# Optimization experiments

Measured on AMD Instinct MI355X. Metric: run time of the kernel, lower is better.

## Reference

```python
import jax, jax.numpy as jnp
import numpy as np
from itertools import permutations

NODE, BATCH, DIM, STEP = 32, 64, 32, 8
E = NODE * (NODE - 1)          # 992 directed edges (all ordered pairs)
K = 3                          # edge types
MSG_HID = 64; MSG_OUT = 64; N_HID = 64; PRED_LEN = 8


def setup_inputs() -> dict:
    key = jax.random.key(0)
    ks = jax.random.split(key, 12)
    es = jnp.asarray(np.array(list(permutations(range(NODE), 2))).T, dtype=jnp.int32)  # [2, E]
    x = jax.random.normal(ks[0], (BATCH, NODE, DIM, STEP), jnp.float32)
    z = jax.nn.softmax(jax.random.normal(ks[1], (BATCH, E, K), jnp.float32), axis=-1)
    p = lambda k, shape: jax.random.normal(k, shape, jnp.float32) * 0.1
    return dict(
        x=x, z=z, es=es,
        nodes_mask=jnp.zeros((NODE,), jnp.float32),
        edges_mask=jnp.zeros((E,), jnp.float32),
        mask=jnp.zeros((1,), jnp.float32),
        msg_W1=p(ks[2], (K, 2 * DIM, MSG_HID)), msg_b1=jnp.zeros((K, MSG_HID), jnp.float32),
        msg_W2=p(ks[3], (K, MSG_HID, MSG_OUT)), msg_b2=jnp.zeros((K, MSG_OUT), jnp.float32),
        out_W1=p(ks[4], (DIM + MSG_OUT, N_HID)), out_b1=jnp.zeros((N_HID,), jnp.float32),
        out_W2=p(ks[5], (N_HID, N_HID)), out_b2=jnp.zeros((N_HID,), jnp.float32),
        out_W3=p(ks[6], (N_HID, DIM)), out_b3=jnp.zeros((DIM,), jnp.float32),
        ge_Wi=p(ks[7], (3, N_HID, N_HID)), ge_bi=jnp.zeros((3, N_HID), jnp.float32),
        ge_Wh=p(ks[8], (3, N_HID, N_HID)), ge_bh=jnp.zeros((3, N_HID), jnp.float32),
        gn_Wi=p(ks[9], (3, N_HID + DIM, N_HID + DIM)), gn_bi=jnp.zeros((3, N_HID + DIM), jnp.float32),
        gn_Wh=p(ks[10], (3, N_HID + DIM, N_HID + DIM)), gn_bh=jnp.zeros((3, N_HID + DIM), jnp.float32),
    )


def _gru(inp, hid, Wi, bi, Wh, bh):
    # GRUX: state defaults to hidden
    r = jax.nn.sigmoid(inp @ Wi[0] + bi[0] + hid @ Wh[0] + bh[0])
    i = jax.nn.sigmoid(inp @ Wi[1] + bi[1] + hid @ Wh[1] + bh[1])
    n = jnp.tanh(inp @ Wi[2] + bi[2] + r * (hid @ Wh[2] + bh[2]))
    return (1.0 - i) * n + i * hid


def _run(x, z, es, msg_W1, msg_b1, msg_W2, msg_b2,
         out_W1, out_b1, out_W2, out_b2, out_W3, out_b3,
         ge_Wi, ge_bi, ge_Wh, ge_bh, gn_Wi, gn_bi, gn_Wh, gn_bh):
    xp = jnp.transpose(x, (1, 0, 3, 2))   # [node, batch, step, dim]
    zp = jnp.transpose(z, (1, 0, 2))      # [E, batch, K]
    col, row = es[0], es[1]               # 'o2i': col,row = es; aggregate at col
    counts = jnp.clip(jax.ops.segment_sum(jnp.ones((E,), x.dtype), col, num_segments=NODE), 1.0)
    h_node = h_edge = None
    x_m = None
    xs = []
    for t in range(STEP + PRED_LEN):
        x_in = xp[:, :, t, :] if t < STEP else x_m   # [node, batch, dim]
        # edge gather: msg = cat([x[row], x[col]])
        msg = jnp.concatenate([x_in[row], x_in[col]], axis=-1)  # [E, b, 2*dim]
        # per-edge-type 2-layer MLP mixture, weighted by z, normalized by K
        h1 = jax.nn.relu(jnp.einsum('ebi,kih->kebh', msg, msg_W1) + msg_b1[:, None, None, :])
        h2 = jax.nn.relu(jnp.einsum('kebh,kho->kebo', h1, msg_W2) + msg_b2[:, None, None, :])
        msgs = jnp.einsum('kebo,ebk->ebo', h2, zp) / K          # [E, b, msg_out]
        if h_edge is not None:
            msgs = _gru(msgs, h_edge, ge_Wi, ge_bi, ge_Wh, ge_bh)
        # scatter-mean to nodes
        agg = jax.ops.segment_sum(msgs, col, num_segments=NODE) / counts[:, None, None]
        cat = jnp.concatenate([x_in, agg], axis=-1)             # [node, b, dim+msg_out]
        if h_node is not None:
            cat = _gru(cat, h_node, gn_Wi, gn_bi, gn_Wh, gn_bh)
        h = jax.nn.relu(cat @ out_W1 + out_b1)
        h = jax.nn.relu(h @ out_W2 + out_b2)
        delta = h @ out_W3 + out_b3
        x_m = x_in + delta
        h_node, h_edge = cat, msgs
        xs.append(x_m)
    x_hat = jnp.transpose(jnp.stack(xs, axis=2), (1, 0, 3, 2))  # [batch, node, dim, T]
    return x_hat


def reference(x, z, es, nodes_mask, edges_mask, mask,
              msg_W1, msg_b1, msg_W2, msg_b2,
              out_W1, out_b1, out_W2, out_b2, out_W3, out_b3,
              ge_Wi, ge_bi, ge_Wh, ge_bh, gn_Wi, gn_bi, gn_Wh, gn_bh):
    x_hat = _run(x, z, es, msg_W1, msg_b1, msg_W2, msg_b2,
                 out_W1, out_b1, out_W2, out_b2, out_W3, out_b3,
                 ge_Wi, ge_bi, ge_Wh, ge_bh, gn_Wi, gn_bi, gn_Wh, gn_bh)
    return (x_hat[:, :, :, -PRED_LEN:], x_hat, x_hat)
```

## Files before the change

### kernel.cpp

```cpp
#include <hip/hip_runtime.h>
#include <hip/hip_bf16.h>

#define NNODE 32
#define NB    64
#define NDIM  32
#define NSTEP 8
#define NE    992
#define NTT   16

typedef __bf16 bf16;
typedef __attribute__((ext_vector_type(8))) __bf16 bf16x8;
typedef __attribute__((ext_vector_type(4))) __bf16 bf16x4;
typedef __attribute__((ext_vector_type(4))) float  f32x4;

__device__ __forceinline__ f32x4 mfma_bf16(bf16x8 a, bf16x8 b, f32x4 c) {
  return __builtin_amdgcn_mfma_f32_16x16x32_bf16(a, b, c, 0, 0, 0);
}
__device__ __forceinline__ float sigm(float x) { return 1.0f / (1.0f + __expf(-x)); }
__device__ __forceinline__ float tanh_f(float x) {
  x = fminf(fmaxf(x, -15.0f), 15.0f);
  float e = __expf(2.0f * x);
  return (e - 1.0f) / (e + 1.0f);
}

__global__ void prep_weights(
    const float* __restrict__ msgW1, const float* __restrict__ msgW2,
    const float* __restrict__ geWi,  const float* __restrict__ geWh,
    const float* __restrict__ gnWi,  const float* __restrict__ gnWh,
    const float* __restrict__ oW1,   const float* __restrict__ oW2,
    const float* __restrict__ oW3,
    bf16* __restrict__ B1, bf16* __restrict__ B2,
    bf16* __restrict__ GI, bf16* __restrict__ GH,
    bf16* __restrict__ GN,
    bf16* __restrict__ OW1s, bf16* __restrict__ OW2s, bf16* __restrict__ OW3s) {
  int u = blockIdx.x * 256 + threadIdx.x;
  if (u < 12288) {
    int k = u >> 12, i = (u >> 6) & 63, h = u & 63;
    int kf = i >> 5, quad = (i >> 3) & 3, j = i & 7;
    int nn = k * 64 + h, nt = nn >> 4, lane = quad * 16 + (nn & 15);
    int slot = ((nt * 2 + kf) * 64 + lane) * 8 + j;
    B1[slot] = (bf16)msgW1[u];
    GI[slot] = (bf16)geWi[u];
    GH[slot] = (bf16)geWh[u];
    int ntl = h >> 4, lane2 = quad * 16 + (h & 15);
    int slot2 = k * 4096 + ((ntl * 2 + kf) * 64 + lane2) * 8 + j;
    B2[slot2] = (bf16)msgW2[u];
  } else if (u < 39936) {
    int v = u - 12288;
    int kk = v / 9216, rem = v % 9216, i = rem / 96, h = rem % 96;
    int kf = i >> 5, loc = i & 31, quad = loc >> 3, j = loc & 7;
    int nn = kk * 96 + h, nt = nn >> 4, lane = quad * 16 + (nn & 15);
    int slot = ((nt * 3 + kf) * 64 + lane) * 8 + j;
    GN[slot]         = (bf16)gnWi[v];
    GN[27648 + slot] = (bf16)gnWh[v];
  } else if (u < 46080) {
    int v = u - 39936; int i = v >> 6, h = v & 63;
    int kf = i >> 5, loc = i & 31, quad = loc >> 3, j = loc & 7;
    int nt = h >> 4, lane = quad * 16 + (h & 15);
    OW1s[((nt * 3 + kf) * 64 + lane) * 8 + j] = (bf16)oW1[v];
  } else if (u < 50176) {
    int v = u - 46080; int i = v >> 6, h = v & 63;
    int kf = i >> 5, quad = (i >> 3) & 3, j = i & 7;
    int nt = h >> 4, lane = quad * 16 + (h & 15);
    OW2s[((nt * 2 + kf) * 64 + lane) * 8 + j] = (bf16)oW2[v];
  } else if (u < 52224) {
    int v = u - 50176; int i = v >> 5, h = v & 31;
    int kf = i >> 5, quad = (i >> 3) & 3, j = i & 7;
    int nt = h >> 4, lane = quad * 16 + (h & 15);
    OW3s[((nt * 2 + kf) * 64 + lane) * 8 + j] = (bf16)oW3[v];
  }
}

__global__ void copy_x(const float* __restrict__ x, float* __restrict__ xf,
                       bf16* __restrict__ xb) {
  int u = blockIdx.x * 256 + threadIdx.x;
  int n = u >> 11, b = (u >> 5) & 63, d = u & 31;
  float v = x[((b * 32 + n) * 32 + d) * 8 + 0];
  xf[u] = v;
  xb[u] = (bf16)v;
}

__global__ __launch_bounds__(256, 2) void edge_step(
    const bf16* __restrict__ xb, const int* __restrict__ es,
    const float* __restrict__ z,
    const bf16* __restrict__ B1, const bf16* __restrict__ B2,
    const float* __restrict__ mb1, const float* __restrict__ mb2,
    const bf16* __restrict__ GI, const bf16* __restrict__ GH,
    const float* __restrict__ gbi, const float* __restrict__ gbh,
    bf16* __restrict__ hed, int t) {
  __shared__ __align__(16) char scrbuf[51200];
  __shared__ float zL[2][64][3];
  __shared__ float biasL[768];
  bf16 (*A)[64][72]   = (bf16(*)[64][72])scrbuf;
  bf16 (*A2)[64][200] = (bf16(*)[64][200])scrbuf;

  int e0 = blockIdx.x * 2, tid = threadIdx.x;
  int c0_ = es[e0],     r0 = es[NE + e0];
  int c1_ = es[e0 + 1], r1 = es[NE + e0 + 1];
  for (int u = tid; u < 768; u += 256)
    biasL[u] = (u < 192) ? mb1[u] : (u < 384) ? mb2[u - 192]
             : (u < 576) ? gbi[u - 384] : gbh[u - 576];
  for (int u = tid; u < 384; u += 256) {
    int pe = u / 192, rem = u % 192, b = rem / 3, k = rem % 3;
    zL[pe][b][k] = z[(b * NE + e0 + pe) * 3 + k];
  }
  for (int u = tid; u < 1024; u += 256) {
    int pe = u >> 9, c = u & 511;
    int b = c >> 3, i8 = c & 7;
    int nrow = pe ? r1 : r0, ncol = pe ? c1_ : c0_;
    const bf16* src = (i8 < 4) ? (xb + nrow * 2048 + b * 32 + i8 * 8)
                               : (xb + ncol * 2048 + b * 32 + (i8 - 4) * 8);
    *(bf16x8*)&A[pe][b][i8 * 8] = *(const bf16x8*)src;
  }
  __syncthreads();
  int wv = tid >> 6, ln = tid & 63, quad = ln >> 4, l16 = ln & 15;
  int m = wv * 16 + l16;
  bf16x8 af[2][2];
#pragma unroll
  for (int pe = 0; pe < 2; pe++)
#pragma unroll
    for (int kf = 0; kf < 2; kf++)
      af[pe][kf] = *(const bf16x8*)&A[pe][m][kf * 32 + quad * 8];
  __syncthreads();
  f32x4 acc[2][12];
#pragma unroll
  for (int pe = 0; pe < 2; pe++)
#pragma unroll
    for (int q = 0; q < 12; q++) { f32x4 zz = {0.f,0.f,0.f,0.f}; acc[pe][q] = zz; }
#pragma unroll
  for (int nt = 0; nt < 12; nt++) {
    bf16x8 w0 = *(const bf16x8*)&B1[(nt * 2 + 0) * 512 + ln * 8];
    bf16x8 w1 = *(const bf16x8*)&B1[(nt * 2 + 1) * 512 + ln * 8];
#pragma unroll
    for (int pe = 0; pe < 2; pe++) {
      acc[pe][nt] = mfma_bf16(af[pe][0], w0, acc[pe][nt]);
      acc[pe][nt] = mfma_bf16(af[pe][1], w1, acc[pe][nt]);
    }
  }
#pragma unroll
  for (int nt = 0; nt < 12; nt++) {
    int n = nt * 16 + l16;
    float bias = biasL[n];
#pragma unroll
    for (int pe = 0; pe < 2; pe++)
#pragma unroll
      for (int r = 0; r < 4; r++) {
        float v = acc[pe][nt][r] + bias;
        A2[pe][wv * 16 + quad * 4 + r][n] = (bf16)(v > 0.f ? v : 0.f);
      }
  }
  __syncthreads();
  bf16x8 a2[2][3][2];
#pragma unroll
  for (int pe = 0; pe < 2; pe++)
#pragma unroll
    for (int kt = 0; kt < 3; kt++)
#pragma unroll
      for (int kf = 0; kf < 2; kf++)
        a2[pe][kt][kf] = *(const bf16x8*)&A2[pe][m][kt * 64 + kf * 32 + quad * 8];
  __syncthreads();
  f32x4 acc2[2][12];
#pragma unroll
  for (int pe = 0; pe < 2; pe++)
#pragma unroll
    for (int q = 0; q < 12; q++) { f32x4 zz = {0.f,0.f,0.f,0.f}; acc2[pe][q] = zz; }
#pragma unroll
  for (int kt = 0; kt < 3; kt++)
#pragma unroll
    for (int nt = 0; nt < 4; nt++) {
      bf16x8 w0 = *(const bf16x8*)&B2[kt * 4096 + (nt * 2 + 0) * 512 + ln * 8];
      bf16x8 w1 = *(const bf16x8*)&B2[kt * 4096 + (nt * 2 + 1) * 512 + ln * 8];
#pragma unroll
      for (int pe = 0; pe < 2; pe++) {
        acc2[pe][kt * 4 + nt] = mfma_bf16(a2[pe][kt][0], w0, acc2[pe][kt * 4 + nt]);
        acc2[pe][kt * 4 + nt] = mfma_bf16(a2[pe][kt][1], w1, acc2[pe][kt * 4 + nt]);
      }
    }
#pragma unroll
  for (int pe = 0; pe < 2; pe++)
#pragma unroll
    for (int r = 0; r < 4; r++) {
      int b = wv * 16 + quad * 4 + r;
      float z0 = zL[pe][b][0], z1 = zL[pe][b][1], z2 = zL[pe][b][2];
#pragma unroll
      for (int nt = 0; nt < 4; nt++) {
        int o = nt * 16 + l16;
        float h0 = acc2[pe][nt][r]     + biasL[192 + o];       h0 = h0 > 0.f ? h0 : 0.f;
        float h1 = acc2[pe][4 + nt][r] + biasL[192 + 64 + o];  h1 = h1 > 0.f ? h1 : 0.f;
        float h2 = acc2[pe][8 + nt][r] + biasL[192 + 128 + o]; h2 = h2 > 0.f ? h2 : 0.f;
        A[pe][b][o] = (bf16)((h0 * z0 + h1 * z1 + h2 * z2) * (1.0f / 3.0f));
      }
    }
  if (t > 0) {
    __syncthreads();
    bf16x8 ai[2][2], ah[2][2];
#pragma unroll
    for (int pe = 0; pe < 2; pe++) {
      const bf16* hrow = hed + (e0 + pe) * 4096 + m * 64;
#pragma unroll
      for (int kf = 0; kf < 2; kf++) {
        ai[pe][kf] = *(const bf16x8*)&A[pe][m][kf * 32 + quad * 8];
        ah[pe][kf] = *(const bf16x8*)(hrow + kf * 32 + quad * 8);
      }
    }
    f32x4 gri[2][8], gni[2][4], gnh[2][4];
#pragma unroll
    for (int pe = 0; pe < 2; pe++) {
#pragma unroll
      for (int q = 0; q < 8; q++) { f32x4 zz = {0.f,0.f,0.f,0.f}; gri[pe][q] = zz; }
#pragma unroll
      for (int q = 0; q < 4; q++) { f32x4 zz = {0.f,0.f,0.f,0.f}; gni[pe][q] = zz; gnh[pe][q] = zz; }
    }
#pragma unroll
    for (int nt = 0; nt < 8; nt++) {
      bf16x8 wi0 = *(const bf16x8*)&GI[(nt * 2 + 0) * 512 + ln * 8];
      bf16x8 wi1 = *(const bf16x8*)&GI[(nt * 2 + 1) * 512 + ln * 8];
      bf16x8 wh0 = *(const bf16x8*)&GH[(nt * 2 + 0) * 512 + ln * 8];
      bf16x8 wh1 = *(const bf16x8*)&GH[(nt * 2 + 1) * 512 + ln * 8];
#pragma unroll
      for (int pe = 0; pe < 2; pe++) {
        gri[pe][nt] = mfma_bf16(ai[pe][0], wi0, gri[pe][nt]);
        gri[pe][nt] = mfma_bf16(ai[pe][1], wi1, gri[pe][nt]);
        gri[pe][nt] = mfma_bf16(ah[pe][0], wh0, gri[pe][nt]);
        gri[pe][nt] = mfma_bf16(ah[pe][1], wh1, gri[pe][nt]);
      }
    }
#pragma unroll
    for (int nt = 8; nt < 12; nt++) {
      bf16x8 wi0 = *(const bf16x8*)&GI[(nt * 2 + 0) * 512 + ln * 8];
      bf16x8 wi1 = *(const bf16x8*)&GI[(nt * 2 + 1) * 512 + ln * 8];
      bf16x8 wh0 = *(const bf16x8*)&GH[(nt * 2 + 0) * 512 + ln * 8];
      bf16x8 wh1 = *(const bf16x8*)&GH[(nt * 2 + 1) * 512 + ln * 8];
#pragma unroll
      for (int pe = 0; pe < 2; pe++) {
        gni[pe][nt - 8] = mfma_bf16(ai[pe][0], wi0, gni[pe][nt - 8]);
        gni[pe][nt - 8] = mfma_bf16(ai[pe][1], wi1, gni[pe][nt - 8]);
        gnh[pe][nt - 8] = mfma_bf16(ah[pe][0], wh0, gnh[pe][nt - 8]);
        gnh[pe][nt - 8] = mfma_bf16(ah[pe][1], wh1, gnh[pe][nt - 8]);
      }
    }
#pragma unroll
    for (int pe = 0; pe < 2; pe++)
#pragma unroll
      for (int r = 0; r < 4; r++) {
        int b = wv * 16 + quad * 4 + r;
#pragma unroll
        for (int nt = 0; nt < 4; nt++) {
          int o = nt * 16 + l16;
          float xr = gri[pe][nt][r]     + biasL[384 + o]      + biasL[576 + o];
          float xi = gri[pe][4 + nt][r] + biasL[384 + 64 + o] + biasL[576 + 64 + o];
          float xn = gni[pe][nt][r] + biasL[384 + 128 + o];
          float hn = gnh[pe][nt][r] + biasL[576 + 128 + o];
          float rg = sigm(xr);
          float ig = sigm(xi);
          float ng = tanh_f(xn + rg * hn);
          float hv = (float)hed[(e0 + pe) * 4096 + b * 64 + o];
          A[pe][b][o] = (bf16)((1.0f - ig) * ng + ig * hv);
        }
      }
  }
  __syncthreads();
  for (int u = tid; u < 1024; u += 256) {
    int pe = u >> 9, c = u & 511;
    int b = c >> 3, j = c & 7;
    *(bf16x8*)(hed + (e0 + pe) * 4096 + b * 64 + j * 8) = *(const bf16x8*)&A[pe][b][j * 8];
  }
}

__global__ __launch_bounds__(256) void node_kernel(
    const float* __restrict__ x, const bf16* __restrict__ hed,
    float* __restrict__ xf, bf16* __restrict__ xb, float* __restrict__ hnode,
    const bf16* __restrict__ GN,
    const float* __restrict__ gnbi, const float* __restrict__ gnbh,
    const bf16* __restrict__ OW1, const float* __restrict__ ob1,
    const bf16* __restrict__ OW2, const float* __restrict__ ob2,
    const bf16* __restrict__ OW3, const float* __restrict__ ob3,
    float* __restrict__ out, int t) {
  __shared__ float aggf[16][64];
  __shared__ float xinf[16][32];
  __shared__ float hvf[16][96];
  __shared__ __align__(16) bf16 c0b[16][112];
  __shared__ __align__(16) bf16 hvb[16][112];
  __shared__ float gsum[2][16][290];
  __shared__ __align__(16) bf16 cnb[16][112];
  __shared__ __align__(16) bf16 s1b[16][112];
  __shared__ __align__(16) bf16 s2b[16][112];
  int nq = blockIdx.x, n = nq >> 2, q = nq & 3;
  int tid = threadIdx.x;
  {
    int r = tid >> 4, o4 = tid & 15;
    const bf16x4* bp = (const bf16x4*)hed + (size_t)n * 31 * 1024 + (q * 16 + r) * 16 + o4;
    float sx = 0.f, sy = 0.f, sz = 0.f, sw = 0.f;
#pragma unroll
    for (int e2 = 0; e2 < 31; e2++) {
      bf16x4 v = bp[e2 * 1024];
      sx += (float)v[0]; sy += (float)v[1]; sz += (float)v[2]; sw += (float)v[3];
    }
    const float inv = 1.0f / 31.0f;
    sx *= inv; sy *= inv; sz *= inv; sw *= inv;
    int o = o4 * 4;
    aggf[r][o] = sx; aggf[r][o + 1] = sy; aggf[r][o + 2] = sz; aggf[r][o + 3] = sw;
    c0b[r][32 + o] = (bf16)sx; c0b[r][33 + o] = (bf16)sy;
    c0b[r][34 + o] = (bf16)sz; c0b[r][35 + o] = (bf16)sw;
  }
  if (tid < 128) {
    int r = tid >> 3, d0 = (tid & 7) * 4;
    int b = q * 16 + r;
#pragma unroll
    for (int k = 0; k < 4; k++) {
      float v = xf[n * 2048 + b * 32 + d0 + k];
      xinf[r][d0 + k] = v;
      c0b[r][d0 + k] = (bf16)v;
    }
  }
  if (t > 0) {
    int r = tid >> 4, cb = (tid & 15) * 6;
    int row = n * 64 + q * 16 + r;
#pragma unroll
    for (int k = 0; k < 6; k++) {
      float v = hnode[row * 96 + cb + k];
      hvf[r][cb + k] = v;
      hvb[r][cb + k] = (bf16)v;
    }
  }
  __syncthreads();
  int wv = tid >> 6, ln = tid & 63, quad = ln >> 4, l16 = ln & 15;
  if (t > 0) {
    int mat = wv >> 1, sel = wv & 1;
    const bf16(*Ab)[112] = mat ? hvb : c0b;
    bf16x8 af[3];
#pragma unroll
    for (int kf = 0; kf < 3; kf++)
      af[kf] = *(const bf16x8*)&Ab[l16][kf * 32 + quad * 8];
    const bf16* W = GN + mat * 27648;
    f32x4 accn[9];
#pragma unroll
    for (int q2 = 0; q2 < 9; q2++) { f32x4 zz = {0.f,0.f,0.f,0.f}; accn[q2] = zz; }
#pragma unroll
    for (int nt2 = 0; nt2 < 9; nt2++) {
      int nt = sel * 9 + nt2;
#pragma unroll
      for (int kf = 0; kf < 3; kf++) {
        bf16x8 bfrag = *(const bf16x8*)&W[((nt * 3 + kf) * 64 + ln) * 8];
        accn[nt2] = mfma_bf16(af[kf], bfrag, accn[nt2]);
      }
    }
#pragma unroll
    for (int nt2 = 0; nt2 < 9; nt2++) {
      int col = (sel * 9 + nt2) * 16 + l16;
#pragma unroll
      for (int rr = 0; rr < 4; rr++)
        gsum[mat][quad * 4 + rr][col] = accn[nt2][rr];
    }
  }
  __syncthreads();
  {
    int r = tid >> 4, cb = (tid & 15) * 6;
    int row = n * 64 + q * 16 + r;
#pragma unroll
    for (int k = 0; k < 6; k++) {
      int c = cb + k;
      float v;
      if (t > 0) {
        float xr = gsum[0][r][c] + gnbi[c] + gsum[1][r][c] + gnbh[c];
        float xi = gsum[0][r][96 + c] + gnbi[96 + c] + gsum[1][r][96 + c] + gnbh[96 + c];
        float xn = gsum[0][r][192 + c] + gnbi[192 + c];
        float hn = gsum[1][r][192 + c] + gnbh[192 + c];
        float rg = sigm(xr);
        float ig = sigm(xi);
        float ng = tanh_f(xn + rg * hn);
        v = (1.0f - ig) * ng + ig * hvf[r][c];
      } else {
        v = (c < 32) ? xinf[r][c] : aggf[r][c - 32];
      }
      cnb[r][c] = (bf16)v;
      hnode[row * 96 + c] = v;
    }
  }
  __syncthreads();
  {
    bf16x8 af[3];
#pragma unroll
    for (int kf = 0; kf < 3; kf++)
      af[kf] = *(const bf16x8*)&cnb[l16][kf * 32 + quad * 8];
    f32x4 accn = {0.f, 0.f, 0.f, 0.f};
#pragma unroll
    for (int kf = 0; kf < 3; kf++) {
      bf16x8 bfrag = *(const bf16x8*)&OW1[((wv * 3 + kf) * 64 + ln) * 8];
      accn = mfma_bf16(af[kf], bfrag, accn);
    }
    int col = wv * 16 + l16;
    float bias = ob1[col];
#pragma unroll
    for (int rr = 0; rr < 4; rr++) {
      float vv = accn[rr] + bias;
      s1b[quad * 4 + rr][col] = (bf16)(vv > 0.f ? vv : 0.f);
    }
  }
  __syncthreads();
  {
    bf16x8 af[2];
#pragma unroll
    for (int kf = 0; kf < 2; kf++)
      af[kf] = *(const bf16x8*)&s1b[l16][kf * 32 + quad * 8];
    f32x4 accn = {0.f, 0.f, 0.f, 0.f};
#pragma unroll
    for (int kf = 0; kf < 2; kf++) {
      bf16x8 bfrag = *(const bf16x8*)&OW2[((wv * 2 + kf) * 64 + ln) * 8];
      accn = mfma_bf16(af[kf], bfrag, accn);
    }
    int col = wv * 16 + l16;
    float bias = ob2[col];
#pragma unroll
    for (int rr = 0; rr < 4; rr++) {
      float vv = accn[rr] + bias;
      s2b[quad * 4 + rr][col] = (bf16)(vv > 0.f ? vv : 0.f);
    }
  }
  __syncthreads();
  if (wv < 2) {
    bf16x8 af[2];
#pragma unroll
    for (int kf = 0; kf < 2; kf++)
      af[kf] = *(const bf16x8*)&s2b[l16][kf * 32 + quad * 8];
    f32x4 accn = {0.f, 0.f, 0.f, 0.f};
#pragma unroll
    for (int kf = 0; kf < 2; kf++) {
      bf16x8 bfrag = *(const bf16x8*)&OW3[((wv * 2 + kf) * 64 + ln) * 8];
      accn = mfma_bf16(af[kf], bfrag, accn);
    }
    int d = wv * 16 + l16;
    float bias = ob3[d];
#pragma unroll
    for (int rr = 0; rr < 4; rr++) {
      int r = quad * 4 + rr;
      int b = q * 16 + r;
      float xm = xinf[r][d] + accn[rr] + bias;
      int base = (b * 32 + n) * 32 + d;
      out[524288 + base * 16 + t] = xm;
      out[1572864 + base * 16 + t] = xm;
      if (t >= NSTEP) out[base * 8 + (t - NSTEP)] = xm;
      float vnext = (t + 1 < NSTEP) ? x[base * 8 + (t + 1)] : xm;
      xf[n * 2048 + b * 32 + d] = vnext;
      xb[n * 2048 + b * 32 + d] = (bf16)vnext;
    }
  }
}

extern "C" void kernel_launch(void* const* d_in, const int* in_sizes, int n_in,
                              void* d_out, int out_size, void* d_ws, size_t ws_size,
                              hipStream_t stream) {
  const float* x     = (const float*)d_in[0];
  const float* z     = (const float*)d_in[1];
  const int*   es    = (const int*)d_in[2];
  const float* msgW1 = (const float*)d_in[6];
  const float* msgb1 = (const float*)d_in[7];
  const float* msgW2 = (const float*)d_in[8];
  const float* msgb2 = (const float*)d_in[9];
  const float* oW1   = (const float*)d_in[10];
  const float* ob1   = (const float*)d_in[11];
  const float* oW2   = (const float*)d_in[12];
  const float* ob2   = (const float*)d_in[13];
  const float* oW3   = (const float*)d_in[14];
  const float* ob3   = (const float*)d_in[15];
  const float* geWi  = (const float*)d_in[16];
  const float* gebi  = (const float*)d_in[17];
  const float* geWh  = (const float*)d_in[18];
  const float* gebh  = (const float*)d_in[19];
  const float* gnWi  = (const float*)d_in[20];
  const float* gnbi  = (const float*)d_in[21];
  const float* gnWh  = (const float*)d_in[22];
  const float* gnbh  = (const float*)d_in[23];
  float* out = (float*)d_out;

  char* p = (char*)d_ws;
  bf16*  hed   = (bf16*)p;   p += (size_t)NE * 4096 * 2;
  float* xf    = (float*)p;  p += 65536 * 4;
  bf16*  xb    = (bf16*)p;   p += 65536 * 2;
  float* hnode = (float*)p;  p += 196608 * 4;
  bf16*  B1sw  = (bf16*)p;   p += 12288 * 2;
  bf16*  B2sw  = (bf16*)p;   p += 12288 * 2;
  bf16*  GIsw  = (bf16*)p;   p += 12288 * 2;
  bf16*  GHsw  = (bf16*)p;   p += 12288 * 2;
  bf16*  GNsw  = (bf16*)p;   p += 55296 * 2;
  bf16*  OW1s  = (bf16*)p;   p += 6144 * 2;
  bf16*  OW2s  = (bf16*)p;   p += 4096 * 2;
  bf16*  OW3s  = (bf16*)p;   p += 2048 * 2;

  prep_weights<<<204, 256, 0, stream>>>(msgW1, msgW2, geWi, geWh, gnWi, gnWh,
                                        oW1, oW2, oW3,
                                        B1sw, B2sw, GIsw, GHsw, GNsw,
                                        OW1s, OW2s, OW3s);
  copy_x<<<256, 256, 0, stream>>>(x, xf, xb);

  for (int t = 0; t < NTT; t++) {
    edge_step<<<NE / 2, 256, 0, stream>>>(xb, es, z, B1sw, B2sw, msgb1, msgb2,
                                          GIsw, GHsw, gebi, gebh, hed, t);
    node_kernel<<<128, 256, 0, stream>>>(x, hed, xf, xb, hnode, GNsw, gnbi, gnbh,
                                         OW1s, ob1, OW2s, ob2, OW3s, ob3,
                                         out, t);
  }
}
```

Baseline: 657.7 us.

## Split edge_step output columns across two wave groups with 512-thread blocks

The edge kernel now runs 8 waves per block instead of 4. Waves are grouped by row (rg) and by column half (cg), and each wave computes half of the output tiles for the message MLP and the edge GRU. This cuts per-wave accumulator registers and serial MFMA chains so more waves can run and hide latency. In exchange, each wave reloads the same A fragments and there is more per-block sync overhead. The launch bound is raised to (512, 4), which constrains registers per thread.

```diff
diff --git a/kernel.cpp b/kernel.cpp
--- a/kernel.cpp
+++ b/kernel.cpp
@@ -80,7 +80,7 @@
   xb[u] = (bf16)v;
 }
 
-__global__ __launch_bounds__(256, 2) void edge_step(
+__global__ __launch_bounds__(512, 4) void edge_step(
     const bf16* __restrict__ xb, const int* __restrict__ es,
     const float* __restrict__ z,
     const bf16* __restrict__ B1, const bf16* __restrict__ B2,
@@ -97,14 +97,14 @@
   int e0 = blockIdx.x * 2, tid = threadIdx.x;
   int c0_ = es[e0],     r0 = es[NE + e0];
   int c1_ = es[e0 + 1], r1 = es[NE + e0 + 1];
-  for (int u = tid; u < 768; u += 256)
+  for (int u = tid; u < 768; u += 512)
     biasL[u] = (u < 192) ? mb1[u] : (u < 384) ? mb2[u - 192]
              : (u < 576) ? gbi[u - 384] : gbh[u - 576];
-  for (int u = tid; u < 384; u += 256) {
+  for (int u = tid; u < 384; u += 512) {
     int pe = u / 192, rem = u % 192, b = rem / 3, k = rem % 3;
     zL[pe][b][k] = z[(b * NE + e0 + pe) * 3 + k];
   }
-  for (int u = tid; u < 1024; u += 256) {
+  for (int u = tid; u < 1024; u += 512) {
     int pe = u >> 9, c = u & 511;
     int b = c >> 3, i8 = c & 7;
     int nrow = pe ? r1 : r0, ncol = pe ? c1_ : c0_;
@@ -114,7 +114,8 @@
   }
   __syncthreads();
   int wv = tid >> 6, ln = tid & 63, quad = ln >> 4, l16 = ln & 15;
-  int m = wv * 16 + l16;
+  int rg = wv & 3, cg = wv >> 2;
+  int m = rg * 16 + l16;
   bf16x8 af[2][2];
 #pragma unroll
   for (int pe = 0; pe < 2; pe++)
@@ -122,72 +123,76 @@
     for (int kf = 0; kf < 2; kf++)
       af[pe][kf] = *(const bf16x8*)&A[pe][m][kf * 32 + quad * 8];
   __syncthreads();
-  f32x4 acc[2][12];
+  f32x4 acc1[2][6];
 #pragma unroll
   for (int pe = 0; pe < 2; pe++)
 #pragma unroll
-    for (int q = 0; q < 12; q++) { f32x4 zz = {0.f,0.f,0.f,0.f}; acc[pe][q] = zz; }
-#pragma unroll
-  for (int nt = 0; nt < 12; nt++) {
+    for (int q = 0; q < 6; q++) { f32x4 zz = {0.f,0.f,0.f,0.f}; acc1[pe][q] = zz; }
+#pragma unroll
+  for (int j = 0; j < 6; j++) {
+    int nt = cg * 6 + j;
     bf16x8 w0 = *(const bf16x8*)&B1[(nt * 2 + 0) * 512 + ln * 8];
     bf16x8 w1 = *(const bf16x8*)&B1[(nt * 2 + 1) * 512 + ln * 8];
 #pragma unroll
     for (int pe = 0; pe < 2; pe++) {
-      acc[pe][nt] = mfma_bf16(af[pe][0], w0, acc[pe][nt]);
-      acc[pe][nt] = mfma_bf16(af[pe][1], w1, acc[pe][nt]);
-    }
-  }
-#pragma unroll
-  for (int nt = 0; nt < 12; nt++) {
+      acc1[pe][j] = mfma_bf16(af[pe][0], w0, acc1[pe][j]);
+      acc1[pe][j] = mfma_bf16(af[pe][1], w1, acc1[pe][j]);
+    }
+  }
+#pragma unroll
+  for (int j = 0; j < 6; j++) {
+    int nt = cg * 6 + j;
     int n = nt * 16 + l16;
     float bias = biasL[n];
 #pragma unroll
     for (int pe = 0; pe < 2; pe++)
 #pragma unroll
       for (int r = 0; r < 4; r++) {
-        float v = acc[pe][nt][r] + bias;
-        A2[pe][wv * 16 + quad * 4 + r][n] = (bf16)(v > 0.f ? v : 0.f);
-      }
-  }
-  __syncthreads();
-  bf16x8 a2[2][3][2];
+        float v = acc1[pe][j][r] + bias;
+        A2[pe][rg * 16 + quad * 4 + r][n] = (bf16)(v > 0.f ? v : 0.f);
+      }
+  }
+  __syncthreads();
+  f32x4 acc2[2][3][2];
 #pragma unroll
   for (int pe = 0; pe < 2; pe++)
 #pragma unroll
     for (int kt = 0; kt < 3; kt++)
 #pragma unroll
+      for (int oi = 0; oi < 2; oi++) { f32x4 zz = {0.f,0.f,0.f,0.f}; acc2[pe][kt][oi] = zz; }
+#pragma unroll
+  for (int kt = 0; kt < 3; kt++) {
+    bf16x8 a2f[2][2];
+#pragma unroll
+    for (int pe = 0; pe < 2; pe++)
+#pragma unroll
       for (int kf = 0; kf < 2; kf++)
-        a2[pe][kt][kf] = *(const bf16x8*)&A2[pe][m][kt * 64 + kf * 32 + quad * 8];
-  __syncthreads();
-  f32x4 acc2[2][12];
+        a2f[pe][kf] = *(const bf16x8*)&A2[pe][m][kt * 64 + kf * 32 + quad * 8];
+#pragma unroll
+    for (int oi = 0; oi < 2; oi++) {
+      int ot = cg * 2 + oi;
+      bf16x8 w0 = *(const bf16x8*)&B2[kt * 4096 + (ot * 2 + 0) * 512 + ln * 8];
+      bf16x8 w1 = *(const bf16x8*)&B2[kt * 4096 + (ot * 2 + 1) * 512 + ln * 8];
+#pragma unroll
+      for (int pe = 0; pe < 2; pe++) {
+        acc2[pe][kt][oi] = mfma_bf16(a2f[pe][0], w0, acc2[pe][kt][oi]);
+        acc2[pe][kt][oi] = mfma_bf16(a2f[pe][1], w1, acc2[pe][kt][oi]);
+      }
+    }
+  }
+  __syncthreads();
 #pragma unroll
   for (int pe = 0; pe < 2; pe++)
 #pragma unroll
-    for (int q = 0; q < 12; q++) { f32x4 zz = {0.f,0.f,0.f,0.f}; acc2[pe][q] = zz; }
-#pragma unroll
-  for (int kt = 0; kt < 3; kt++)
-#pragma unroll
-    for (int nt = 0; nt < 4; nt++) {
-      bf16x8 w0 = *(const bf16x8*)&B2[kt * 4096 + (nt * 2 + 0) * 512 + ln * 8];
-      bf16x8 w1 = *(const bf16x8*)&B2[kt * 4096 + (nt * 2 + 1) * 512 + ln * 8];
-#pragma unroll
-      for (int pe = 0; pe < 2; pe++) {
-        acc2[pe][kt * 4 + nt] = mfma_bf16(a2[pe][kt][0], w0, acc2[pe][kt * 4 + nt]);
-        acc2[pe][kt * 4 + nt] = mfma_bf16(a2[pe][kt][1], w1, acc2[pe][kt * 4 + nt]);
-      }
-    }
-#pragma unroll
-  for (int pe = 0; pe < 2; pe++)
-#pragma unroll
     for (int r = 0; r < 4; r++) {
-      int b = wv * 16 + quad * 4 + r;
+      int b = rg * 16 + quad * 4 + r;
       float z0 = zL[pe][b][0], z1 = zL[pe][b][1], z2 = zL[pe][b][2];
 #pragma unroll
-      for (int nt = 0; nt < 4; nt++) {
-        int o = nt * 16 + l16;
-        float h0 = acc2[pe][nt][r]     + biasL[192 + o];       h0 = h0 > 0.f ? h0 : 0.f;
-        float h1 = acc2[pe][4 + nt][r] + biasL[192 + 64 + o];  h1 = h1 > 0.f ? h1 : 0.f;
-        float h2 = acc2[pe][8 + nt][r] + biasL[192 + 128 + o]; h2 = h2 > 0.f ? h2 : 0.f;
+      for (int oi = 0; oi < 2; oi++) {
+        int o = (cg * 2 + oi) * 16 + l16;
+        float h0 = acc2[pe][0][oi][r] + biasL[192 + o];       h0 = h0 > 0.f ? h0 : 0.f;
+        float h1 = acc2[pe][1][oi][r] + biasL[192 + 64 + o];  h1 = h1 > 0.f ? h1 : 0.f;
+        float h2 = acc2[pe][2][oi][r] + biasL[192 + 128 + o]; h2 = h2 > 0.f ? h2 : 0.f;
         A[pe][b][o] = (bf16)((h0 * z0 + h1 * z1 + h2 * z2) * (1.0f / 3.0f));
       }
     }
@@ -203,64 +208,66 @@
         ah[pe][kf] = *(const bf16x8*)(hrow + kf * 32 + quad * 8);
       }
     }
-    f32x4 gri[2][8], gni[2][4], gnh[2][4];
-#pragma unroll
-    for (int pe = 0; pe < 2; pe++) {
-#pragma unroll
-      for (int q = 0; q < 8; q++) { f32x4 zz = {0.f,0.f,0.f,0.f}; gri[pe][q] = zz; }
-#pragma unroll
-      for (int q = 0; q < 4; q++) { f32x4 zz = {0.f,0.f,0.f,0.f}; gni[pe][q] = zz; gnh[pe][q] = zz; }
-    }
-#pragma unroll
-    for (int nt = 0; nt < 8; nt++) {
-      bf16x8 wi0 = *(const bf16x8*)&GI[(nt * 2 + 0) * 512 + ln * 8];
-      bf16x8 wi1 = *(const bf16x8*)&GI[(nt * 2 + 1) * 512 + ln * 8];
-      bf16x8 wh0 = *(const bf16x8*)&GH[(nt * 2 + 0) * 512 + ln * 8];
-      bf16x8 wh1 = *(const bf16x8*)&GH[(nt * 2 + 1) * 512 + ln * 8];
+#pragma unroll
+    for (int oi = 0; oi < 2; oi++) {
+      int ot = cg * 2 + oi;
+      f32x4 gr[2], gi2[2], gni2[2], gnh2[2];
 #pragma unroll
       for (int pe = 0; pe < 2; pe++) {
-        gri[pe][nt] = mfma_bf16(ai[pe][0], wi0, gri[pe][nt]);
-        gri[pe][nt] = mfma_bf16(ai[pe][1], wi1, gri[pe][nt]);
-        gri[pe][nt] = mfma_bf16(ah[pe][0], wh0, gri[pe][nt]);
-        gri[pe][nt] = mfma_bf16(ah[pe][1], wh1, gri[pe][nt]);
-      }
-    }
-#pragma unroll
-    for (int nt = 8; nt < 12; nt++) {
-      bf16x8 wi0 = *(const bf16x8*)&GI[(nt * 2 + 0) * 512 + ln * 8];
-      bf16x8 wi1 = *(const bf16x8*)&GI[(nt * 2 + 1) * 512 + ln * 8];
-      bf16x8 wh0 = *(const bf16x8*)&GH[(nt * 2 + 0) * 512 + ln * 8];
-      bf16x8 wh1 = *(const bf16x8*)&GH[(nt * 2 + 1) * 512 + ln * 8];
-#pragma unroll
-      for (int pe = 0; pe < 2; pe++) {
-        gni[pe][nt - 8] = mfma_bf16(ai[pe][0], wi0, gni[pe][nt - 8]);
-        gni[pe][nt - 8] = mfma_bf16(ai[pe][1], wi1, gni[pe][nt - 8]);
-        gnh[pe][nt - 8] = mfma_bf16(ah[pe][0], wh0, gnh[pe][nt - 8]);
-        gnh[pe][nt - 8] = mfma_bf16(ah[pe][1], wh1, gnh[pe][nt - 8]);
-      }
-    }
-#pragma unroll
-    for (int pe = 0; pe < 2; pe++)
-#pragma unroll
-      for (int r = 0; r < 4; r++) {
-        int b = wv * 16 + quad * 4 + r;
-#pragma unroll
-        for (int nt = 0; nt < 4; nt++) {
-          int o = nt * 16 + l16;
-          float xr = gri[pe][nt][r]     + biasL[384 + o]      + biasL[576 + o];
-          float xi = gri[pe][4 + nt][r] + biasL[384 + 64 + o] + biasL[576 + 64 + o];
-          float xn = gni[pe][nt][r] + biasL[384 + 128 + o];
-          float hn = gnh[pe][nt][r] + biasL[576 + 128 + o];
-          float rg = sigm(xr);
-          float ig = sigm(xi);
-          float ng = tanh_f(xn + rg * hn);
-          float hv = (float)hed[(e0 + pe) * 4096 + b * 64 + o];
+        f32x4 zz = {0.f,0.f,0.f,0.f};
+        gr[pe] = zz; gi2[pe] = zz; gni2[pe] = zz; gnh2[pe] = zz;
+      }
+#pragma unroll
+      for (int g = 0; g < 2; g++) {
+        int nt = g * 4 + ot;
+        bf16x8 wi0 = *(const bf16x8*)&GI[(nt * 2 + 0) * 512 + ln * 8];
+        bf16x8 wi1 = *(const bf16x8*)&GI[(nt * 2 + 1) * 512 + ln * 8];
+        bf16x8 wh0 = *(const bf16x8*)&GH[(nt * 2 + 0) * 512 + ln * 8];
+        bf16x8 wh1 = *(const bf16x8*)&GH[(nt * 2 + 1) * 512 + ln * 8];
+#pragma unroll
+        for (int pe = 0; pe < 2; pe++) {
+          f32x4 a = g ? gi2[pe] : gr[pe];
+          a = mfma_bf16(ai[pe][0], wi0, a);
+          a = mfma_bf16(ai[pe][1], wi1, a);
+          a = mfma_bf16(ah[pe][0], wh0, a);
+          a = mfma_bf16(ah[pe][1], wh1, a);
+          if (g) gi2[pe] = a; else gr[pe] = a;
+        }
+      }
+      {
+        int nt = 8 + ot;
+        bf16x8 wi0 = *(const bf16x8*)&GI[(nt * 2 + 0) * 512 + ln * 8];
+        bf16x8 wi1 = *(const bf16x8*)&GI[(nt * 2 + 1) * 512 + ln * 8];
+        bf16x8 wh0 = *(const bf16x8*)&GH[(nt * 2 + 0) * 512 + ln * 8];
+        bf16x8 wh1 = *(const bf16x8*)&GH[(nt * 2 + 1) * 512 + ln * 8];
+#pragma unroll
+        for (int pe = 0; pe < 2; pe++) {
+          gni2[pe] = mfma_bf16(ai[pe][0], wi0, gni2[pe]);
+          gni2[pe] = mfma_bf16(ai[pe][1], wi1, gni2[pe]);
+          gnh2[pe] = mfma_bf16(ah[pe][0], wh0, gnh2[pe]);
+          gnh2[pe] = mfma_bf16(ah[pe][1], wh1, gnh2[pe]);
+        }
+      }
+#pragma unroll
+      for (int pe = 0; pe < 2; pe++)
+#pragma unroll
+        for (int r = 0; r < 4; r++) {
+          int b = rg * 16 + quad * 4 + r;
+          int o = ot * 16 + l16;
+          float xr = gr[pe][r]   + biasL[384 + o]       + biasL[576 + o];
+          float xi = gi2[pe][r]  + biasL[384 + 64 + o]  + biasL[576 + 64 + o];
+          float xn = gni2[pe][r] + biasL[384 + 128 + o];
+          float hn = gnh2[pe][r] + biasL[576 + 128 + o];
+          float rgt = sigm(xr);
+          float ig  = sigm(xi);
+          float ng  = tanh_f(xn + rgt * hn);
+          float hv  = (float)hed[(e0 + pe) * 4096 + b * 64 + o];
           A[pe][b][o] = (bf16)((1.0f - ig) * ng + ig * hv);
         }
-      }
-  }
-  __syncthreads();
-  for (int u = tid; u < 1024; u += 256) {
+    }
+  }
+  __syncthreads();
+  for (int u = tid; u < 1024; u += 512) {
     int pe = u >> 9, c = u & 511;
     int b = c >> 3, j = c & 7;
     *(bf16x8*)(hed + (e0 + pe) * 4096 + b * 64 + j * 8) = *(const bf16x8*)&A[pe][b][j * 8];
@@ -494,7 +501,7 @@
   copy_x<<<256, 256, 0, stream>>>(x, xf, xb);
 
   for (int t = 0; t < NTT; t++) {
-    edge_step<<<NE / 2, 256, 0, stream>>>(xb, es, z, B1sw, B2sw, msgb1, msgb2,
+    edge_step<<<NE / 2, 512, 0, stream>>>(xb, es, z, B1sw, B2sw, msgb1, msgb2,
                                           GIsw, GHsw, gebi, gebh, hed, t);
     node_kernel<<<128, 256, 0, stream>>>(x, hed, xf, xb, hnode, GNsw, gnbi, gnbh,
                                          OW1s, ob1, OW2s, ob2, OW3s, ob3,
```

Result: faster. 614.2 us (-6.6%).

## Restructure edge kernel to one edge per block with per-wave LDS and no block barriers

Applied to the files above, without the earlier changes.

Each edge_step block now handles one edge instead of two, doubling the grid and allowing four blocks per CU through launch bounds. Each wave owns a private 16-row LDS slice, so block-wide __syncthreads are replaced by an lgkmcnt wait fence. The z-weighted mix of the three message MLPs is now accumulated in registers per k-slice instead of keeping all twelve accumulator tiles live. GRU gate bias loads now come straight from global memory, not staged in LDS. The aim is lower register pressure, less LDS and fewer barriers for more occupancy and latency hiding, at the cost of re-reading weights per block for half as many edges.

```diff
diff --git a/kernel.cpp b/kernel.cpp
--- a/kernel.cpp
+++ b/kernel.cpp
@@ -21,6 +21,10 @@
   x = fminf(fmaxf(x, -15.0f), 15.0f);
   float e = __expf(2.0f * x);
   return (e - 1.0f) / (e + 1.0f);
+}
+__device__ __forceinline__ void lds_fence() {
+  asm volatile("s_waitcnt lgkmcnt(0)" ::: "memory");
+  __builtin_amdgcn_sched_barrier(0);
 }
 
 __global__ void prep_weights(
@@ -80,7 +84,7 @@
   xb[u] = (bf16)v;
 }
 
-__global__ __launch_bounds__(256, 2) void edge_step(
+__global__ __launch_bounds__(256, 4) void edge_step(
     const bf16* __restrict__ xb, const int* __restrict__ es,
     const float* __restrict__ z,
     const bf16* __restrict__ B1, const bf16* __restrict__ B2,
@@ -88,182 +92,153 @@
     const bf16* __restrict__ GI, const bf16* __restrict__ GH,
     const float* __restrict__ gbi, const float* __restrict__ gbh,
     bf16* __restrict__ hed, int t) {
-  __shared__ __align__(16) char scrbuf[51200];
-  __shared__ float zL[2][64][3];
-  __shared__ float biasL[768];
-  bf16 (*A)[64][72]   = (bf16(*)[64][72])scrbuf;
-  bf16 (*A2)[64][200] = (bf16(*)[64][200])scrbuf;
-
-  int e0 = blockIdx.x * 2, tid = threadIdx.x;
-  int c0_ = es[e0],     r0 = es[NE + e0];
-  int c1_ = es[e0 + 1], r1 = es[NE + e0 + 1];
-  for (int u = tid; u < 768; u += 256)
-    biasL[u] = (u < 192) ? mb1[u] : (u < 384) ? mb2[u - 192]
-             : (u < 576) ? gbi[u - 384] : gbh[u - 576];
-  for (int u = tid; u < 384; u += 256) {
-    int pe = u / 192, rem = u % 192, b = rem / 3, k = rem % 3;
-    zL[pe][b][k] = z[(b * NE + e0 + pe) * 3 + k];
-  }
-  for (int u = tid; u < 1024; u += 256) {
-    int pe = u >> 9, c = u & 511;
-    int b = c >> 3, i8 = c & 7;
-    int nrow = pe ? r1 : r0, ncol = pe ? c1_ : c0_;
-    const bf16* src = (i8 < 4) ? (xb + nrow * 2048 + b * 32 + i8 * 8)
-                               : (xb + ncol * 2048 + b * 32 + (i8 - 4) * 8);
-    *(bf16x8*)&A[pe][b][i8 * 8] = *(const bf16x8*)src;
-  }
-  __syncthreads();
+  __shared__ __align__(16) bf16 sl[4][16][216];
+  int e = blockIdx.x, tid = threadIdx.x;
   int wv = tid >> 6, ln = tid & 63, quad = ln >> 4, l16 = ln & 15;
-  int m = wv * 16 + l16;
-  bf16x8 af[2][2];
-#pragma unroll
-  for (int pe = 0; pe < 2; pe++)
-#pragma unroll
-    for (int kf = 0; kf < 2; kf++)
-      af[pe][kf] = *(const bf16x8*)&A[pe][m][kf * 32 + quad * 8];
-  __syncthreads();
-  f32x4 acc[2][12];
-#pragma unroll
-  for (int pe = 0; pe < 2; pe++)
-#pragma unroll
-    for (int q = 0; q < 12; q++) { f32x4 zz = {0.f,0.f,0.f,0.f}; acc[pe][q] = zz; }
+  int cn = es[e], rn = es[NE + e];
+  int b0 = wv * 16;
+  bf16 (*S)[216] = sl[wv];
+
+  bf16x8 af0 = *(const bf16x8*)(xb + rn * 2048 + (b0 + l16) * 32 + quad * 8);
+  bf16x8 af1 = *(const bf16x8*)(xb + cn * 2048 + (b0 + l16) * 32 + quad * 8);
+  float zv[4][3];
+#pragma unroll
+  for (int rr = 0; rr < 4; rr++) {
+    int b = b0 + quad * 4 + rr;
+#pragma unroll
+    for (int k = 0; k < 3; k++) zv[rr][k] = z[(b * NE + e) * 3 + k];
+  }
+
+  f32x4 acc1[12];
+#pragma unroll
+  for (int nt = 0; nt < 12; nt++) { f32x4 zz = {0.f,0.f,0.f,0.f}; acc1[nt] = zz; }
 #pragma unroll
   for (int nt = 0; nt < 12; nt++) {
     bf16x8 w0 = *(const bf16x8*)&B1[(nt * 2 + 0) * 512 + ln * 8];
     bf16x8 w1 = *(const bf16x8*)&B1[(nt * 2 + 1) * 512 + ln * 8];
-#pragma unroll
-    for (int pe = 0; pe < 2; pe++) {
-      acc[pe][nt] = mfma_bf16(af[pe][0], w0, acc[pe][nt]);
-      acc[pe][nt] = mfma_bf16(af[pe][1], w1, acc[pe][nt]);
-    }
+    acc1[nt] = mfma_bf16(af0, w0, acc1[nt]);
+    acc1[nt] = mfma_bf16(af1, w1, acc1[nt]);
   }
 #pragma unroll
   for (int nt = 0; nt < 12; nt++) {
-    int n = nt * 16 + l16;
-    float bias = biasL[n];
-#pragma unroll
-    for (int pe = 0; pe < 2; pe++)
-#pragma unroll
-      for (int r = 0; r < 4; r++) {
-        float v = acc[pe][nt][r] + bias;
-        A2[pe][wv * 16 + quad * 4 + r][n] = (bf16)(v > 0.f ? v : 0.f);
-      }
-  }
-  __syncthreads();
-  bf16x8 a2[2][3][2];
-#pragma unroll
-  for (int pe = 0; pe < 2; pe++)
-#pragma unroll
-    for (int kt = 0; kt < 3; kt++)
-#pragma unroll
-      for (int kf = 0; kf < 2; kf++)
-        a2[pe][kt][kf] = *(const bf16x8*)&A2[pe][m][kt * 64 + kf * 32 + quad * 8];
-  __syncthreads();
-  f32x4 acc2[2][12];
-#pragma unroll
-  for (int pe = 0; pe < 2; pe++)
-#pragma unroll
-    for (int q = 0; q < 12; q++) { f32x4 zz = {0.f,0.f,0.f,0.f}; acc2[pe][q] = zz; }
-#pragma unroll
-  for (int kt = 0; kt < 3; kt++)
+    float bias = mb1[nt * 16 + l16];
+#pragma unroll
+    for (int rr = 0; rr < 4; rr++) {
+      float v = acc1[nt][rr] + bias;
+      S[quad * 4 + rr][nt * 16 + l16] = (bf16)(v > 0.f ? v : 0.f);
+    }
+  }
+  lds_fence();
+
+  f32x4 mix[4];
+#pragma unroll
+  for (int nt = 0; nt < 4; nt++) { f32x4 zz = {0.f,0.f,0.f,0.f}; mix[nt] = zz; }
+#pragma unroll
+  for (int kt = 0; kt < 3; kt++) {
+    bf16x8 a20 = *(const bf16x8*)&S[l16][kt * 64 + quad * 8];
+    bf16x8 a21 = *(const bf16x8*)&S[l16][kt * 64 + 32 + quad * 8];
+    f32x4 a2c[4];
+#pragma unroll
+    for (int nt = 0; nt < 4; nt++) { f32x4 zz = {0.f,0.f,0.f,0.f}; a2c[nt] = zz; }
 #pragma unroll
     for (int nt = 0; nt < 4; nt++) {
       bf16x8 w0 = *(const bf16x8*)&B2[kt * 4096 + (nt * 2 + 0) * 512 + ln * 8];
       bf16x8 w1 = *(const bf16x8*)&B2[kt * 4096 + (nt * 2 + 1) * 512 + ln * 8];
-#pragma unroll
-      for (int pe = 0; pe < 2; pe++) {
-        acc2[pe][kt * 4 + nt] = mfma_bf16(a2[pe][kt][0], w0, acc2[pe][kt * 4 + nt]);
-        acc2[pe][kt * 4 + nt] = mfma_bf16(a2[pe][kt][1], w1, acc2[pe][kt * 4 + nt]);
-      }
-    }
-#pragma unroll
-  for (int pe = 0; pe < 2; pe++)
-#pragma unroll
-    for (int r = 0; r < 4; r++) {
-      int b = wv * 16 + quad * 4 + r;
-      float z0 = zL[pe][b][0], z1 = zL[pe][b][1], z2 = zL[pe][b][2];
-#pragma unroll
-      for (int nt = 0; nt < 4; nt++) {
-        int o = nt * 16 + l16;
-        float h0 = acc2[pe][nt][r]     + biasL[192 + o];       h0 = h0 > 0.f ? h0 : 0.f;
-        float h1 = acc2[pe][4 + nt][r] + biasL[192 + 64 + o];  h1 = h1 > 0.f ? h1 : 0.f;
-        float h2 = acc2[pe][8 + nt][r] + biasL[192 + 128 + o]; h2 = h2 > 0.f ? h2 : 0.f;
-        A[pe][b][o] = (bf16)((h0 * z0 + h1 * z1 + h2 * z2) * (1.0f / 3.0f));
-      }
-    }
-  if (t > 0) {
-    __syncthreads();
-    bf16x8 ai[2][2], ah[2][2];
-#pragma unroll
-    for (int pe = 0; pe < 2; pe++) {
-      const bf16* hrow = hed + (e0 + pe) * 4096 + m * 64;
-#pragma unroll
-      for (int kf = 0; kf < 2; kf++) {
-        ai[pe][kf] = *(const bf16x8*)&A[pe][m][kf * 32 + quad * 8];
-        ah[pe][kf] = *(const bf16x8*)(hrow + kf * 32 + quad * 8);
-      }
-    }
-    f32x4 gri[2][8], gni[2][4], gnh[2][4];
-#pragma unroll
-    for (int pe = 0; pe < 2; pe++) {
-#pragma unroll
-      for (int q = 0; q < 8; q++) { f32x4 zz = {0.f,0.f,0.f,0.f}; gri[pe][q] = zz; }
-#pragma unroll
-      for (int q = 0; q < 4; q++) { f32x4 zz = {0.f,0.f,0.f,0.f}; gni[pe][q] = zz; gnh[pe][q] = zz; }
-    }
-#pragma unroll
-    for (int nt = 0; nt < 8; nt++) {
-      bf16x8 wi0 = *(const bf16x8*)&GI[(nt * 2 + 0) * 512 + ln * 8];
-      bf16x8 wi1 = *(const bf16x8*)&GI[(nt * 2 + 1) * 512 + ln * 8];
-      bf16x8 wh0 = *(const bf16x8*)&GH[(nt * 2 + 0) * 512 + ln * 8];
-      bf16x8 wh1 = *(const bf16x8*)&GH[(nt * 2 + 1) * 512 + ln * 8];
-#pragma unroll
-      for (int pe = 0; pe < 2; pe++) {
-        gri[pe][nt] = mfma_bf16(ai[pe][0], wi0, gri[pe][nt]);
-        gri[pe][nt] = mfma_bf16(ai[pe][1], wi1, gri[pe][nt]);
-        gri[pe][nt] = mfma_bf16(ah[pe][0], wh0, gri[pe][nt]);
-        gri[pe][nt] = mfma_bf16(ah[pe][1], wh1, gri[pe][nt]);
-      }
-    }
-#pragma unroll
-    for (int nt = 8; nt < 12; nt++) {
-      bf16x8 wi0 = *(const bf16x8*)&GI[(nt * 2 + 0) * 512 + ln * 8];
-      bf16x8 wi1 = *(const bf16x8*)&GI[(nt * 2 + 1) * 512 + ln * 8];
-      bf16x8 wh0 = *(const bf16x8*)&GH[(nt * 2 + 0) * 512 + ln * 8];
-      bf16x8 wh1 = *(const bf16x8*)&GH[(nt * 2 + 1) * 512 + ln * 8];
-#pragma unroll
-      for (int pe = 0; pe < 2; pe++) {
-        gni[pe][nt - 8] = mfma_bf16(ai[pe][0], wi0, gni[pe][nt - 8]);
-        gni[pe][nt - 8] = mfma_bf16(ai[pe][1], wi1, gni[pe][nt - 8]);
-        gnh[pe][nt - 8] = mfma_bf16(ah[pe][0], wh0, gnh[pe][nt - 8]);
-        gnh[pe][nt - 8] = mfma_bf16(ah[pe][1], wh1, gnh[pe][nt - 8]);
-      }
-    }
-#pragma unroll
-    for (int pe = 0; pe < 2; pe++)
-#pragma unroll
-      for (int r = 0; r < 4; r++) {
-        int b = wv * 16 + quad * 4 + r;
-#pragma unroll
-        for (int nt = 0; nt < 4; nt++) {
-          int o = nt * 16 + l16;
-          float xr = gri[pe][nt][r]     + biasL[384 + o]      + biasL[576 + o];
-          float xi = gri[pe][4 + nt][r] + biasL[384 + 64 + o] + biasL[576 + 64 + o];
-          float xn = gni[pe][nt][r] + biasL[384 + 128 + o];
-          float hn = gnh[pe][nt][r] + biasL[576 + 128 + o];
-          float rg = sigm(xr);
-          float ig = sigm(xi);
-          float ng = tanh_f(xn + rg * hn);
-          float hv = (float)hed[(e0 + pe) * 4096 + b * 64 + o];
-          A[pe][b][o] = (bf16)((1.0f - ig) * ng + ig * hv);
-        }
-      }
-  }
-  __syncthreads();
-  for (int u = tid; u < 1024; u += 256) {
-    int pe = u >> 9, c = u & 511;
-    int b = c >> 3, j = c & 7;
-    *(bf16x8*)(hed + (e0 + pe) * 4096 + b * 64 + j * 8) = *(const bf16x8*)&A[pe][b][j * 8];
+      a2c[nt] = mfma_bf16(a20, w0, a2c[nt]);
+      a2c[nt] = mfma_bf16(a21, w1, a2c[nt]);
+    }
+#pragma unroll
+    for (int nt = 0; nt < 4; nt++) {
+      float bias = mb2[kt * 64 + nt * 16 + l16];
+#pragma unroll
+      for (int rr = 0; rr < 4; rr++) {
+        float h = a2c[nt][rr] + bias;
+        h = h > 0.f ? h : 0.f;
+        mix[nt][rr] = fmaf(h, zv[rr][kt], mix[nt][rr]);
+      }
+    }
+  }
+  const float inv3 = 1.0f / 3.0f;
+
+  if (t == 0) {
+#pragma unroll
+    for (int nt = 0; nt < 4; nt++)
+#pragma unroll
+      for (int rr = 0; rr < 4; rr++)
+        S[quad * 4 + rr][128 + nt * 16 + l16] = (bf16)(mix[nt][rr] * inv3);
+    lds_fence();
+    bf16x8 h0 = *(const bf16x8*)&S[l16][128 + quad * 16];
+    bf16x8 h1 = *(const bf16x8*)&S[l16][128 + quad * 16 + 8];
+    bf16* dst = hed + e * 4096 + (b0 + l16) * 64 + quad * 16;
+    *(bf16x8*)dst = h0;
+    *(bf16x8*)(dst + 8) = h1;
+  } else {
+#pragma unroll
+    for (int nt = 0; nt < 4; nt++)
+#pragma unroll
+      for (int rr = 0; rr < 4; rr++)
+        S[quad * 4 + rr][64 + nt * 16 + l16] = (bf16)(mix[nt][rr] * inv3);
+    const bf16* hrow = hed + e * 4096 + (b0 + l16) * 64;
+    bf16x8 ah0 = *(const bf16x8*)(hrow + quad * 8);
+    bf16x8 ah1 = *(const bf16x8*)(hrow + 32 + quad * 8);
+    *(bf16x8*)&S[l16][128 + quad * 8] = ah0;
+    *(bf16x8*)&S[l16][160 + quad * 8] = ah1;
+    lds_fence();
+    bf16x8 ai0 = *(const bf16x8*)&S[l16][64 + quad * 8];
+    bf16x8 ai1 = *(const bf16x8*)&S[l16][96 + quad * 8];
+#pragma unroll
+    for (int nt = 0; nt < 4; nt++) {
+      f32x4 gr = {0.f,0.f,0.f,0.f}, gi = {0.f,0.f,0.f,0.f};
+      f32x4 gn = {0.f,0.f,0.f,0.f}, gh = {0.f,0.f,0.f,0.f};
+      {
+        bf16x8 wi0 = *(const bf16x8*)&GI[(nt * 2 + 0) * 512 + ln * 8];
+        bf16x8 wi1 = *(const bf16x8*)&GI[(nt * 2 + 1) * 512 + ln * 8];
+        bf16x8 wh0 = *(const bf16x8*)&GH[(nt * 2 + 0) * 512 + ln * 8];
+        bf16x8 wh1 = *(const bf16x8*)&GH[(nt * 2 + 1) * 512 + ln * 8];
+        gr = mfma_bf16(ai0, wi0, gr); gr = mfma_bf16(ai1, wi1, gr);
+        gr = mfma_bf16(ah0, wh0, gr); gr = mfma_bf16(ah1, wh1, gr);
+      }
+      {
+        int a = 4 + nt;
+        bf16x8 wi0 = *(const bf16x8*)&GI[(a * 2 + 0) * 512 + ln * 8];
+        bf16x8 wi1 = *(const bf16x8*)&GI[(a * 2 + 1) * 512 + ln * 8];
+        bf16x8 wh0 = *(const bf16x8*)&GH[(a * 2 + 0) * 512 + ln * 8];
+        bf16x8 wh1 = *(const bf16x8*)&GH[(a * 2 + 1) * 512 + ln * 8];
+        gi = mfma_bf16(ai0, wi0, gi); gi = mfma_bf16(ai1, wi1, gi);
+        gi = mfma_bf16(ah0, wh0, gi); gi = mfma_bf16(ah1, wh1, gi);
+      }
+      {
+        int a = 8 + nt;
+        bf16x8 wi0 = *(const bf16x8*)&GI[(a * 2 + 0) * 512 + ln * 8];
+        bf16x8 wi1 = *(const bf16x8*)&GI[(a * 2 + 1) * 512 + ln * 8];
+        bf16x8 wh0 = *(const bf16x8*)&GH[(a * 2 + 0) * 512 + ln * 8];
+        bf16x8 wh1 = *(const bf16x8*)&GH[(a * 2 + 1) * 512 + ln * 8];
+        gn = mfma_bf16(ai0, wi0, gn); gn = mfma_bf16(ai1, wi1, gn);
+        gh = mfma_bf16(ah0, wh0, gh); gh = mfma_bf16(ah1, wh1, gh);
+      }
+      int o = nt * 16 + l16;
+      float bir = gbi[o],       bhr = gbh[o];
+      float bii = gbi[64 + o],  bhi = gbh[64 + o];
+      float bin = gbi[128 + o], bhn = gbh[128 + o];
+#pragma unroll
+      for (int rr = 0; rr < 4; rr++) {
+        float xr = gr[rr] + bir + bhr;
+        float xi = gi[rr] + bii + bhi;
+        float xn = gn[rr] + bin;
+        float hn = gh[rr] + bhn;
+        float rg = sigm(xr);
+        float ig = sigm(xi);
+        float ng = tanh_f(xn + rg * hn);
+        float hv = (float)S[quad * 4 + rr][128 + o];
+        S[quad * 4 + rr][64 + o] = (bf16)((1.0f - ig) * ng + ig * hv);
+      }
+    }
+    lds_fence();
+    bf16x8 h0 = *(const bf16x8*)&S[l16][64 + quad * 16];
+    bf16x8 h1 = *(const bf16x8*)&S[l16][64 + quad * 16 + 8];
+    bf16* dst = hed + e * 4096 + (b0 + l16) * 64 + quad * 16;
+    *(bf16x8*)dst = h0;
+    *(bf16x8*)(dst + 8) = h1;
   }
 }
 
@@ -379,15 +354,15 @@
   }
   __syncthreads();
   {
-    bf16x8 af[3];
+    bf16x8 af3[3];
 #pragma unroll
     for (int kf = 0; kf < 3; kf++)
-      af[kf] = *(const bf16x8*)&cnb[l16][kf * 32 + quad * 8];
+      af3[kf] = *(const bf16x8*)&cnb[l16][kf * 32 + quad * 8];
     f32x4 accn = {0.f, 0.f, 0.f, 0.f};
 #pragma unroll
     for (int kf = 0; kf < 3; kf++) {
       bf16x8 bfrag = *(const bf16x8*)&OW1[((wv * 3 + kf) * 64 + ln) * 8];
-      accn = mfma_bf16(af[kf], bfrag, accn);
+      accn = mfma_bf16(af3[kf], bfrag, accn);
     }
     int col = wv * 16 + l16;
     float bias = ob1[col];
@@ -399,15 +374,15 @@
   }
   __syncthreads();
   {
-    bf16x8 af[2];
+    bf16x8 af2[2];
 #pragma unroll
     for (int kf = 0; kf < 2; kf++)
-      af[kf] = *(const bf16x8*)&s1b[l16][kf * 32 + quad * 8];
+      af2[kf] = *(const bf16x8*)&s1b[l16][kf * 32 + quad * 8];
     f32x4 accn = {0.f, 0.f, 0.f, 0.f};
 #pragma unroll
     for (int kf = 0; kf < 2; kf++) {
       bf16x8 bfrag = *(const bf16x8*)&OW2[((wv * 2 + kf) * 64 + ln) * 8];
-      accn = mfma_bf16(af[kf], bfrag, accn);
+      accn = mfma_bf16(af2[kf], bfrag, accn);
     }
     int col = wv * 16 + l16;
     float bias = ob2[col];
@@ -419,15 +394,15 @@
   }
   __syncthreads();
   if (wv < 2) {
-    bf16x8 af[2];
+    bf16x8 af2[2];
 #pragma unroll
     for (int kf = 0; kf < 2; kf++)
-      af[kf] = *(const bf16x8*)&s2b[l16][kf * 32 + quad * 8];
+      af2[kf] = *(const bf16x8*)&s2b[l16][kf * 32 + quad * 8];
     f32x4 accn = {0.f, 0.f, 0.f, 0.f};
 #pragma unroll
     for (int kf = 0; kf < 2; kf++) {
       bf16x8 bfrag = *(const bf16x8*)&OW3[((wv * 2 + kf) * 64 + ln) * 8];
-      accn = mfma_bf16(af[kf], bfrag, accn);
+      accn = mfma_bf16(af2[kf], bfrag, accn);
     }
     int d = wv * 16 + l16;
     float bias = ob3[d];
@@ -494,8 +469,8 @@
   copy_x<<<256, 256, 0, stream>>>(x, xf, xb);
 
   for (int t = 0; t < NTT; t++) {
-    edge_step<<<NE / 2, 256, 0, stream>>>(xb, es, z, B1sw, B2sw, msgb1, msgb2,
-                                          GIsw, GHsw, gebi, gebh, hed, t);
+    edge_step<<<NE, 256, 0, stream>>>(xb, es, z, B1sw, B2sw, msgb1, msgb2,
+                                      GIsw, GHsw, gebi, gebh, hed, t);
     node_kernel<<<128, 256, 0, stream>>>(x, hed, xf, xb, hnode, GNsw, gnbi, gnbh,
                                          OW1s, ob1, OW2s, ob2, OW3s, ob3,
                                          out, t);
```

New measurement: 658.6 us. About the same (+0.1%).
